# Kernel optimization log

Hardware: AMD Instinct MI355X
Metric: run time of the kernel (lower is better)

## Reference

```python
import jax, jax.numpy as jnp
import numpy as np

ENC_H, PRED_H, JOINT_H, NUM_CLASSES = 768, 320, 320, 34


def setup_inputs() -> dict:
    key = jax.random.key(0)
    ks = jax.random.split(key, 8)
    B, T, U = 8, 512, 128
    s = lambda fan_in: 1.0 / np.sqrt(fan_in)
    return {
        "enc_out": jax.random.normal(ks[0], (B, T, ENC_H), dtype=jnp.float32),
        "pred_out": jax.random.normal(ks[1], (B, U, PRED_H), dtype=jnp.float32),
        "enc_w": jax.random.uniform(ks[2], (JOINT_H, ENC_H), jnp.float32, -s(ENC_H), s(ENC_H)),
        "enc_b": jax.random.uniform(ks[3], (JOINT_H,), jnp.float32, -s(ENC_H), s(ENC_H)),
        "pred_w": jax.random.uniform(ks[4], (JOINT_H, PRED_H), jnp.float32, -s(PRED_H), s(PRED_H)),
        "pred_b": jax.random.uniform(ks[5], (JOINT_H,), jnp.float32, -s(PRED_H), s(PRED_H)),
        "out_w": jax.random.uniform(ks[6], (NUM_CLASSES, JOINT_H), jnp.float32, -s(JOINT_H), s(JOINT_H)),
        "out_b": jax.random.uniform(ks[7], (NUM_CLASSES,), jnp.float32, -s(JOINT_H), s(JOINT_H)),
    }


def reference(enc_out, pred_out, enc_w, enc_b, pred_w, pred_b, out_w, out_b):
    # project encoder and predictor streams to joint_hidden
    f = jnp.einsum("bte,he->bth", enc_out, enc_w) + enc_b   # [B,T,H]
    g = jnp.einsum("bup,hp->buh", pred_out, pred_w) + pred_b  # [B,U,H]
    # broadcast-sum over (T,U), ReLU, output projection
    joint = jax.nn.relu(f[:, :, None, :] + g[:, None, :, :])  # [B,T,U,H]
    logits = jnp.einsum("btuh,ch->btuc", joint, out_w) + out_b  # [B,T,U,C]
    return logits
```

## Files before the change

### kernel.cpp

```cpp
#include <hip/hip_runtime.h>
#include <hip/hip_bf16.h>
#include <hip/hip_fp16.h>


typedef _Float16 f16x8 __attribute__((ext_vector_type(8)));
typedef __fp16   fp16x2 __attribute__((ext_vector_type(2)));
typedef float    f32x4 __attribute__((ext_vector_type(4)));
typedef int      i32x4 __attribute__((ext_vector_type(4)));

#define B_ 8
#define T_ 512
#define U_ 128
#define H_ 320
#define C_ 34

__device__ inline f16x8 pack8(f32x4 a, f32x4 b) {
    union { fp16x2 h[4]; f16x8 v; } u;
    u.h[0] = __builtin_amdgcn_cvt_pkrtz(a[0], a[1]);
    u.h[1] = __builtin_amdgcn_cvt_pkrtz(a[2], a[3]);
    u.h[2] = __builtin_amdgcn_cvt_pkrtz(b[0], b[1]);
    u.h[3] = __builtin_amdgcn_cvt_pkrtz(b[2], b[3]);
    return u.v;
}

__global__ __launch_bounds__(256, 4)
void proj_fused(const float* __restrict__ enc_out, const float* __restrict__ enc_w,
                const float* __restrict__ enc_b, const float* __restrict__ pred_out,
                const float* __restrict__ pred_w, const float* __restrict__ pred_b,
                _Float16* __restrict__ F, _Float16* __restrict__ G) {
    __shared__ _Float16 As[2][64 * 40];
    __shared__ _Float16 Ws[2][64 * 40];

    int blk = blockIdx.x;
    const float *A, *W, *bias;
    _Float16* Out;
    int K, mt, nt;
    if (blk < 320) {
        A = enc_out; W = enc_w; bias = enc_b; Out = F; K = 768;
        mt = blk & 63; nt = blk >> 6;
    } else {
        blk -= 320;
        A = pred_out; W = pred_w; bias = pred_b; Out = G; K = 320;
        mt = blk & 15; nt = blk >> 4;
    }
    const int bm = mt * 64;
    const int bn = nt * 64;

    const int tid = threadIdx.x;
    const int l   = tid & 63;
    const int w   = tid >> 6;
    const int wm  = (w >> 1) * 32;
    const int wn  = (w & 1) * 32;
    const int q   = l >> 4;
    const int r16 = l & 15;

    const int srow = tid >> 2;
    const int scol = (tid & 3) * 8;

    f32x4 acc[2][2] = {};

    const float* arow = A + (size_t)(bm + srow) * K + scol;
    const float* wrow = W + (size_t)(bn + srow) * K + scol;

    f32x4 a0 = *(const f32x4*)(arow);
    f32x4 a1 = *(const f32x4*)(arow + 4);
    f32x4 w0 = *(const f32x4*)(wrow);
    f32x4 w1 = *(const f32x4*)(wrow + 4);

    int p = 0;
    for (int k0 = 0; k0 < K; k0 += 32) {
        *(f16x8*)&As[p][srow * 40 + scol] = pack8(a0, a1);
        *(f16x8*)&Ws[p][srow * 40 + scol] = pack8(w0, w1);

        if (k0 + 32 < K) {
            a0 = *(const f32x4*)(arow + k0 + 32);
            a1 = *(const f32x4*)(arow + k0 + 36);
            w0 = *(const f32x4*)(wrow + k0 + 32);
            w1 = *(const f32x4*)(wrow + k0 + 36);
        }

        __syncthreads();

        f16x8 afr0 = *(const f16x8*)&As[p][(wm + r16) * 40 + q * 8];
        f16x8 afr1 = *(const f16x8*)&As[p][(wm + 16 + r16) * 40 + q * 8];
        f16x8 bfr0 = *(const f16x8*)&Ws[p][(wn + r16) * 40 + q * 8];
        f16x8 bfr1 = *(const f16x8*)&Ws[p][(wn + 16 + r16) * 40 + q * 8];

        acc[0][0] = __builtin_amdgcn_mfma_f32_16x16x32_f16(afr0, bfr0, acc[0][0], 0, 0, 0);
        acc[0][1] = __builtin_amdgcn_mfma_f32_16x16x32_f16(afr0, bfr1, acc[0][1], 0, 0, 0);
        acc[1][0] = __builtin_amdgcn_mfma_f32_16x16x32_f16(afr1, bfr0, acc[1][0], 0, 0, 0);
        acc[1][1] = __builtin_amdgcn_mfma_f32_16x16x32_f16(afr1, bfr1, acc[1][1], 0, 0, 0);
        p ^= 1;
    }

#pragma unroll
    for (int mrep = 0; mrep < 2; ++mrep) {
#pragma unroll
        for (int nrep = 0; nrep < 2; ++nrep) {
            int col  = bn + wn + nrep * 16 + r16;
            float bv = bias[col];
#pragma unroll
            for (int rr = 0; rr < 4; ++rr) {
                int row = bm + wm + mrep * 16 + q * 4 + rr;
                Out[(size_t)row * H_ + col] = (_Float16)(acc[mrep][nrep][rr] + bv);
            }
        }
    }
}

__global__ __launch_bounds__(256, 2)
void joint_kernel(const _Float16* __restrict__ F, const _Float16* __restrict__ G,
                  const float* __restrict__ out_w, const float* __restrict__ out_b,
                  float* __restrict__ out) {
    __shared__ _Float16 glds[16 * 328];

    const int tid = threadIdx.x;
    const int l   = tid & 63;
    const int w   = tid >> 6;
    const int q   = l >> 4;
    const int r16 = l & 15;
    const int tc  = blockIdx.x;
    const int ut  = blockIdx.y;
    const int b   = blockIdx.z;
    const int u0  = ut * 16;

    {
        const _Float16* gsrc = G + ((size_t)b * U_ + u0) * H_;
        for (int i = tid; i < 16 * 40; i += 256) {
            int row = i / 40;
            int c8  = (i - row * 40) * 8;
            *(i32x4*)&glds[row * 328 + c8] = *(const i32x4*)(gsrc + row * H_ + c8);
        }
    }

    f16x8 bfr[3][10];
    float ob[3];
#pragma unroll
    for (int nt = 0; nt < 3; ++nt) {
        const int n = nt * 16 + r16;
        const bool valid = (n < C_);
        const float* wr = out_w + (size_t)n * H_;
        ob[nt] = valid ? out_b[n] : 0.f;
#pragma unroll
        for (int s = 0; s < 10; ++s) {
            f16x8 v = {};
            if (valid) {
                f32x4 x0 = *(const f32x4*)(wr + s * 32 + q * 8);
                f32x4 x1 = *(const f32x4*)(wr + s * 32 + q * 8 + 4);
                v = pack8(x0, x1);
            }
            bfr[nt][s] = v;
        }
    }

    __syncthreads();

    const int tbase = tc * 64 + w * 16;
    for (int tt = 0; tt < 16; ++tt) {
        const int t = tbase + tt;
        const _Float16* frow = F + ((size_t)b * T_ + t) * H_;

        f32x4 acc0 = {}, acc1 = {}, acc2 = {};
#pragma unroll
        for (int s = 0; s < 10; ++s) {
            f16x8 fv = *(const f16x8*)(frow + s * 32 + q * 8);
            f16x8 gv = *(const f16x8*)&glds[r16 * 328 + s * 32 + q * 8];
            f16x8 jv = fv + gv;
            const f16x8 fz = {};
            jv = __builtin_elementwise_max(jv, fz);
            acc0 = __builtin_amdgcn_mfma_f32_16x16x32_f16(jv, bfr[0][s], acc0, 0, 0, 0);
            acc1 = __builtin_amdgcn_mfma_f32_16x16x32_f16(jv, bfr[1][s], acc1, 0, 0, 0);
            acc2 = __builtin_amdgcn_mfma_f32_16x16x32_f16(jv, bfr[2][s], acc2, 0, 0, 0);
        }

        float* orow = out + (((size_t)b * T_ + t) * U_ + u0) * C_;
#pragma unroll
        for (int rr = 0; rr < 4; ++rr) {
            const int m = q * 4 + rr;
            orow[m * C_ + r16]      = acc0[rr] + ob[0];
            orow[m * C_ + 16 + r16] = acc1[rr] + ob[1];
            if (r16 < 2)
                orow[m * C_ + 32 + r16] = acc2[rr] + ob[2];
        }
    }
}

extern "C" void kernel_launch(void* const* d_in, const int* in_sizes, int n_in,
                              void* d_out, int out_size, void* d_ws, size_t ws_size,
                              hipStream_t stream) {
    const float* enc_out  = (const float*)d_in[0];
    const float* pred_out = (const float*)d_in[1];
    const float* enc_w    = (const float*)d_in[2];
    const float* enc_b    = (const float*)d_in[3];
    const float* pred_w   = (const float*)d_in[4];
    const float* pred_b   = (const float*)d_in[5];
    const float* out_w    = (const float*)d_in[6];
    const float* out_b    = (const float*)d_in[7];
    float* out = (float*)d_out;

    char* ws = (char*)d_ws;
    _Float16* F = (_Float16*)ws;
    _Float16* G = (_Float16*)(ws + (size_t)4096 * 320 * 2);

    proj_fused<<<400, 256, 0, stream>>>(enc_out, enc_w, enc_b,
                                        pred_out, pred_w, pred_b, F, G);
    joint_kernel<<<dim3(8, 8, 8), 256, 0, stream>>>(F, G, out_w, out_b, out);
}
```

Before: 51.12 us.

## Merge projection and joint kernels into one cooperative persistent kernel with grid sync

```diff
diff --git a/kernel.cpp b/kernel.cpp
--- a/kernel.cpp
+++ b/kernel.cpp
@@ -1,6 +1,8 @@
 #include <hip/hip_runtime.h>
-#include <hip/hip_bf16.h>
 #include <hip/hip_fp16.h>
+#include <hip/hip_cooperative_groups.h>
+
+namespace cg = cooperative_groups;
 
 
 typedef _Float16 f16x8 __attribute__((ext_vector_type(8)));
@@ -23,164 +25,163 @@
     return u.v;
 }
 
-__global__ __launch_bounds__(256, 4)
-void proj_fused(const float* __restrict__ enc_out, const float* __restrict__ enc_w,
+__global__ __launch_bounds__(256)
+void fused_rnnt(const float* __restrict__ enc_out, const float* __restrict__ enc_w,
                 const float* __restrict__ enc_b, const float* __restrict__ pred_out,
                 const float* __restrict__ pred_w, const float* __restrict__ pred_b,
-                _Float16* __restrict__ F, _Float16* __restrict__ G) {
-    __shared__ _Float16 As[2][64 * 40];
-    __shared__ _Float16 Ws[2][64 * 40];
-
-    int blk = blockIdx.x;
-    const float *A, *W, *bias;
-    _Float16* Out;
-    int K, mt, nt;
-    if (blk < 320) {
-        A = enc_out; W = enc_w; bias = enc_b; Out = F; K = 768;
-        mt = blk & 63; nt = blk >> 6;
-    } else {
-        blk -= 320;
-        A = pred_out; W = pred_w; bias = pred_b; Out = G; K = 320;
-        mt = blk & 15; nt = blk >> 4;
-    }
-    const int bm = mt * 64;
-    const int bn = nt * 64;
-
-    const int tid = threadIdx.x;
-    const int l   = tid & 63;
-    const int w   = tid >> 6;
-    const int wm  = (w >> 1) * 32;
-    const int wn  = (w & 1) * 32;
-    const int q   = l >> 4;
-    const int r16 = l & 15;
-
-    const int srow = tid >> 2;
-    const int scol = (tid & 3) * 8;
-
-    f32x4 acc[2][2] = {};
-
-    const float* arow = A + (size_t)(bm + srow) * K + scol;
-    const float* wrow = W + (size_t)(bn + srow) * K + scol;
-
-    f32x4 a0 = *(const f32x4*)(arow);
-    f32x4 a1 = *(const f32x4*)(arow + 4);
-    f32x4 w0 = *(const f32x4*)(wrow);
-    f32x4 w1 = *(const f32x4*)(wrow + 4);
-
-    int p = 0;
-    for (int k0 = 0; k0 < K; k0 += 32) {
-        *(f16x8*)&As[p][srow * 40 + scol] = pack8(a0, a1);
-        *(f16x8*)&Ws[p][srow * 40 + scol] = pack8(w0, w1);
-
-        if (k0 + 32 < K) {
-            a0 = *(const f32x4*)(arow + k0 + 32);
-            a1 = *(const f32x4*)(arow + k0 + 36);
-            w0 = *(const f32x4*)(wrow + k0 + 32);
-            w1 = *(const f32x4*)(wrow + k0 + 36);
-        }
-
-        __syncthreads();
-
-        f16x8 afr0 = *(const f16x8*)&As[p][(wm + r16) * 40 + q * 8];
-        f16x8 afr1 = *(const f16x8*)&As[p][(wm + 16 + r16) * 40 + q * 8];
-        f16x8 bfr0 = *(const f16x8*)&Ws[p][(wn + r16) * 40 + q * 8];
-        f16x8 bfr1 = *(const f16x8*)&Ws[p][(wn + 16 + r16) * 40 + q * 8];
-
-        acc[0][0] = __builtin_amdgcn_mfma_f32_16x16x32_f16(afr0, bfr0, acc[0][0], 0, 0, 0);
-        acc[0][1] = __builtin_amdgcn_mfma_f32_16x16x32_f16(afr0, bfr1, acc[0][1], 0, 0, 0);
-        acc[1][0] = __builtin_amdgcn_mfma_f32_16x16x32_f16(afr1, bfr0, acc[1][0], 0, 0, 0);
-        acc[1][1] = __builtin_amdgcn_mfma_f32_16x16x32_f16(afr1, bfr1, acc[1][1], 0, 0, 0);
-        p ^= 1;
-    }
-
-#pragma unroll
-    for (int mrep = 0; mrep < 2; ++mrep) {
-#pragma unroll
-        for (int nrep = 0; nrep < 2; ++nrep) {
-            int col  = bn + wn + nrep * 16 + r16;
-            float bv = bias[col];
-#pragma unroll
-            for (int rr = 0; rr < 4; ++rr) {
-                int row = bm + wm + mrep * 16 + q * 4 + rr;
-                Out[(size_t)row * H_ + col] = (_Float16)(acc[mrep][nrep][rr] + bv);
-            }
-        }
-    }
-}
-
-__global__ __launch_bounds__(256, 2)
-void joint_kernel(const _Float16* __restrict__ F, const _Float16* __restrict__ G,
-                  const float* __restrict__ out_w, const float* __restrict__ out_b,
-                  float* __restrict__ out) {
-    __shared__ _Float16 glds[16 * 328];
+                const float* __restrict__ out_w, const float* __restrict__ out_b,
+                _Float16* __restrict__ F, _Float16* __restrict__ G,
+                float* __restrict__ out) {
+    __shared__ _Float16 smem[10240];
+    _Float16* glds = smem;
 
     const int tid = threadIdx.x;
     const int l   = tid & 63;
     const int w   = tid >> 6;
     const int q   = l >> 4;
     const int r16 = l & 15;
-    const int tc  = blockIdx.x;
-    const int ut  = blockIdx.y;
-    const int b   = blockIdx.z;
-    const int u0  = ut * 16;
-
-    {
+
+    const int wm = (w >> 1) * 32;
+    const int wn = (w & 1) * 32;
+    const int srow = tid >> 2;
+    const int scol = (tid & 3) * 8;
+
+    for (int tile = blockIdx.x; tile < 400; tile += gridDim.x) {
+        const float *A, *W, *bias;
+        _Float16* Out;
+        int K, mt, nt;
+        if (tile < 320) {
+            A = enc_out; W = enc_w; bias = enc_b; Out = F; K = 768;
+            mt = tile & 63; nt = tile >> 6;
+        } else {
+            int bl = tile - 320;
+            A = pred_out; W = pred_w; bias = pred_b; Out = G; K = 320;
+            mt = bl & 15; nt = bl >> 4;
+        }
+        const int bm = mt * 64;
+        const int bn = nt * 64;
+
+        _Float16 (*As)[2560] = (_Float16(*)[2560])smem;
+        _Float16 (*Ws)[2560] = (_Float16(*)[2560])(smem + 5120);
+
+        f32x4 acc[2][2] = {};
+        const float* arow = A + (size_t)(bm + srow) * K + scol;
+        const float* wrow = W + (size_t)(bn + srow) * K + scol;
+
+        f32x4 a0 = *(const f32x4*)(arow);
+        f32x4 a1 = *(const f32x4*)(arow + 4);
+        f32x4 w0 = *(const f32x4*)(wrow);
+        f32x4 w1 = *(const f32x4*)(wrow + 4);
+
+        __syncthreads();
+
+        int p = 0;
+        for (int k0 = 0; k0 < K; k0 += 32) {
+            *(f16x8*)&As[p][srow * 40 + scol] = pack8(a0, a1);
+            *(f16x8*)&Ws[p][srow * 40 + scol] = pack8(w0, w1);
+
+            if (k0 + 32 < K) {
+                a0 = *(const f32x4*)(arow + k0 + 32);
+                a1 = *(const f32x4*)(arow + k0 + 36);
+                w0 = *(const f32x4*)(wrow + k0 + 32);
+                w1 = *(const f32x4*)(wrow + k0 + 36);
+            }
+
+            __syncthreads();
+
+            f16x8 afr0 = *(const f16x8*)&As[p][(wm + r16) * 40 + q * 8];
+            f16x8 afr1 = *(const f16x8*)&As[p][(wm + 16 + r16) * 40 + q * 8];
+            f16x8 bfr0 = *(const f16x8*)&Ws[p][(wn + r16) * 40 + q * 8];
+            f16x8 bfr1 = *(const f16x8*)&Ws[p][(wn + 16 + r16) * 40 + q * 8];
+
+            acc[0][0] = __builtin_amdgcn_mfma_f32_16x16x32_f16(afr0, bfr0, acc[0][0], 0, 0, 0);
+            acc[0][1] = __builtin_amdgcn_mfma_f32_16x16x32_f16(afr0, bfr1, acc[0][1], 0, 0, 0);
+            acc[1][0] = __builtin_amdgcn_mfma_f32_16x16x32_f16(afr1, bfr0, acc[1][0], 0, 0, 0);
+            acc[1][1] = __builtin_amdgcn_mfma_f32_16x16x32_f16(afr1, bfr1, acc[1][1], 0, 0, 0);
+            p ^= 1;
+        }
+
+#pragma unroll
+        for (int mrep = 0; mrep < 2; ++mrep) {
+#pragma unroll
+            for (int nrep = 0; nrep < 2; ++nrep) {
+                int col  = bn + wn + nrep * 16 + r16;
+                float bv = bias[col];
+#pragma unroll
+                for (int rr = 0; rr < 4; ++rr) {
+                    int row = bm + wm + mrep * 16 + q * 4 + rr;
+                    Out[(size_t)row * H_ + col] = (_Float16)(acc[mrep][nrep][rr] + bv);
+                }
+            }
+        }
+    }
+
+    cg::this_grid().sync();
+
+    for (int jt = blockIdx.x; jt < 512; jt += gridDim.x) {
+        const int tc = jt & 7;
+        const int ut = (jt >> 3) & 7;
+        const int b  = jt >> 6;
+        const int u0 = ut * 16;
+
+        __syncthreads();
+
         const _Float16* gsrc = G + ((size_t)b * U_ + u0) * H_;
         for (int i = tid; i < 16 * 40; i += 256) {
             int row = i / 40;
             int c8  = (i - row * 40) * 8;
             *(i32x4*)&glds[row * 328 + c8] = *(const i32x4*)(gsrc + row * H_ + c8);
         }
-    }
-
-    f16x8 bfr[3][10];
-    float ob[3];
-#pragma unroll
-    for (int nt = 0; nt < 3; ++nt) {
-        const int n = nt * 16 + r16;
-        const bool valid = (n < C_);
-        const float* wr = out_w + (size_t)n * H_;
-        ob[nt] = valid ? out_b[n] : 0.f;
-#pragma unroll
-        for (int s = 0; s < 10; ++s) {
-            f16x8 v = {};
-            if (valid) {
-                f32x4 x0 = *(const f32x4*)(wr + s * 32 + q * 8);
-                f32x4 x1 = *(const f32x4*)(wr + s * 32 + q * 8 + 4);
-                v = pack8(x0, x1);
-            }
-            bfr[nt][s] = v;
-        }
-    }
-
-    __syncthreads();
-
-    const int tbase = tc * 64 + w * 16;
-    for (int tt = 0; tt < 16; ++tt) {
-        const int t = tbase + tt;
-        const _Float16* frow = F + ((size_t)b * T_ + t) * H_;
-
-        f32x4 acc0 = {}, acc1 = {}, acc2 = {};
-#pragma unroll
-        for (int s = 0; s < 10; ++s) {
-            f16x8 fv = *(const f16x8*)(frow + s * 32 + q * 8);
-            f16x8 gv = *(const f16x8*)&glds[r16 * 328 + s * 32 + q * 8];
-            f16x8 jv = fv + gv;
-            const f16x8 fz = {};
-            jv = __builtin_elementwise_max(jv, fz);
-            acc0 = __builtin_amdgcn_mfma_f32_16x16x32_f16(jv, bfr[0][s], acc0, 0, 0, 0);
-            acc1 = __builtin_amdgcn_mfma_f32_16x16x32_f16(jv, bfr[1][s], acc1, 0, 0, 0);
-            acc2 = __builtin_amdgcn_mfma_f32_16x16x32_f16(jv, bfr[2][s], acc2, 0, 0, 0);
-        }
-
-        float* orow = out + (((size_t)b * T_ + t) * U_ + u0) * C_;
-#pragma unroll
-        for (int rr = 0; rr < 4; ++rr) {
-            const int m = q * 4 + rr;
-            orow[m * C_ + r16]      = acc0[rr] + ob[0];
-            orow[m * C_ + 16 + r16] = acc1[rr] + ob[1];
-            if (r16 < 2)
-                orow[m * C_ + 32 + r16] = acc2[rr] + ob[2];
+
+        f16x8 bfr[3][10];
+        float ob[3];
+#pragma unroll
+        for (int nt = 0; nt < 3; ++nt) {
+            const int n = nt * 16 + r16;
+            const bool valid = (n < C_);
+            const float* wr = out_w + (size_t)n * H_;
+            ob[nt] = valid ? out_b[n] : 0.f;
+#pragma unroll
+            for (int s = 0; s < 10; ++s) {
+                f16x8 v = {};
+                if (valid) {
+                    f32x4 x0 = *(const f32x4*)(wr + s * 32 + q * 8);
+                    f32x4 x1 = *(const f32x4*)(wr + s * 32 + q * 8 + 4);
+                    v = pack8(x0, x1);
+                }
+                bfr[nt][s] = v;
+            }
+        }
+
+        __syncthreads();
+
+        const int tbase = tc * 64 + w * 16;
+        for (int tt = 0; tt < 16; ++tt) {
+            const int t = tbase + tt;
+            const _Float16* frow = F + ((size_t)b * T_ + t) * H_;
+
+            f32x4 acc0 = {}, acc1 = {}, acc2 = {};
+#pragma unroll
+            for (int s = 0; s < 10; ++s) {
+                f16x8 fv = *(const f16x8*)(frow + s * 32 + q * 8);
+                f16x8 gv = *(const f16x8*)&glds[r16 * 328 + s * 32 + q * 8];
+                f16x8 jv = fv + gv;
+                const f16x8 fz = {};
+                jv = __builtin_elementwise_max(jv, fz);
+                acc0 = __builtin_amdgcn_mfma_f32_16x16x32_f16(jv, bfr[0][s], acc0, 0, 0, 0);
+                acc1 = __builtin_amdgcn_mfma_f32_16x16x32_f16(jv, bfr[1][s], acc1, 0, 0, 0);
+                acc2 = __builtin_amdgcn_mfma_f32_16x16x32_f16(jv, bfr[2][s], acc2, 0, 0, 0);
+            }
+
+            float* orow = out + (((size_t)b * T_ + t) * U_ + u0) * C_;
+#pragma unroll
+            for (int rr = 0; rr < 4; ++rr) {
+                const int m = q * 4 + rr;
+                orow[m * C_ + r16]      = acc0[rr] + ob[0];
+                orow[m * C_ + 16 + r16] = acc1[rr] + ob[1];
+                if (r16 < 2)
+                    orow[m * C_ + 32 + r16] = acc2[rr] + ob[2];
+            }
         }
     }
 }
@@ -202,7 +203,15 @@
     _Float16* F = (_Float16*)ws;
     _Float16* G = (_Float16*)(ws + (size_t)4096 * 320 * 2);
 
-    proj_fused<<<400, 256, 0, stream>>>(enc_out, enc_w, enc_b,
-                                        pred_out, pred_w, pred_b, F, G);
-    joint_kernel<<<dim3(8, 8, 8), 256, 0, stream>>>(F, G, out_w, out_b, out);
+    int maxb_per_cu = 0;
+    hipOccupancyMaxActiveBlocksPerMultiprocessor(&maxb_per_cu, fused_rnnt, 256, 0);
+    if (maxb_per_cu < 1) maxb_per_cu = 1;
+    int grid = maxb_per_cu * 256;
+    if (grid > 512) grid = 512;
+
+    void* args[] = {(void*)&enc_out, (void*)&enc_w, (void*)&enc_b,
+                    (void*)&pred_out, (void*)&pred_w, (void*)&pred_b,
+                    (void*)&out_w, (void*)&out_b,
+                    (void*)&F, (void*)&G, (void*)&out};
+    hipLaunchCooperativeKernel(fused_rnnt, dim3(grid), dim3(256), args, 0, stream);
 }
```

Result: slower. 112.4 us (+119.9%).
